# Kernel tuning notes

Measured on AMD Instinct MI355X. Metric: run time of the kernel, lower is better.

## Reference

```python
import jax, jax.numpy as jnp
from jax import lax
import numpy as np

PRE_NMS_TOPN = 6000
POST_NMS_TOPN = 1000  # used as max_output_size_per_class and max_total_size
IOU_THR = 0.7
BATCH = 16
TOTAL_ANCHORS = 147456  # 128*128*9


def setup_inputs() -> dict:
    key = jax.random.key(0)
    k1, k2, k3, k4 = jax.random.split(key, 4)
    B, A = BATCH, TOTAL_ANCHORS
    rpn_bbox_deltas = jax.random.normal(k1, (B, A, 4), jnp.float32) * 0.1
    rpn_labels = jax.random.normal(k2, (B, A), jnp.float32)
    # well-formed anchors in [y1,x1,y2,x2] normalized coords
    tl = jax.random.uniform(k3, (A, 2), jnp.float32, 0.0, 0.9)
    wh = jax.random.uniform(k4, (A, 2), jnp.float32, 0.02, 0.12)
    anchors = jnp.concatenate([tl, tl + wh], axis=-1)
    variances = jnp.array([0.1, 0.1, 0.2, 0.2], jnp.float32)
    return {"rpn_bbox_deltas": rpn_bbox_deltas, "rpn_labels": rpn_labels,
            "anchors": anchors, "variances": variances}


def _decode(anchors, deltas):
    # anchors: (..., A, 4) [y1,x1,y2,x2]; deltas: (..., A, 4) [dy,dx,dh,dw]
    aw = anchors[..., 3] - anchors[..., 1]
    ah = anchors[..., 2] - anchors[..., 0]
    acx = anchors[..., 1] + 0.5 * aw
    acy = anchors[..., 0] + 0.5 * ah
    bw = jnp.exp(deltas[..., 3]) * aw
    bh = jnp.exp(deltas[..., 2]) * ah
    bcx = deltas[..., 1] * aw + acx
    bcy = deltas[..., 0] * ah + acy
    y1 = bcy - 0.5 * bh
    x1 = bcx - 0.5 * bw
    y2 = bh + y1
    x2 = bw + x1
    return jnp.stack([y1, x1, y2, x2], axis=-1)


def _pairwise_iou(b):
    # b: (N, 4) [y1,x1,y2,x2] -> (N, N)
    y1, x1, y2, x2 = b[:, 0], b[:, 1], b[:, 2], b[:, 3]
    area = (y2 - y1) * (x2 - x1)
    iy1 = jnp.maximum(y1[:, None], y1[None, :])
    ix1 = jnp.maximum(x1[:, None], x1[None, :])
    iy2 = jnp.minimum(y2[:, None], y2[None, :])
    ix2 = jnp.minimum(x2[:, None], x2[None, :])
    inter = jnp.maximum(iy2 - iy1, 0.0) * jnp.maximum(ix2 - ix1, 0.0)
    union = area[:, None] + area[None, :] - inter
    return inter / jnp.maximum(union, 1e-9)


def _nms_keep(boxes_sorted):
    # greedy NMS on score-descending boxes; returns bool keep mask (N,)
    n = boxes_sorted.shape[0]
    iou = _pairwise_iou(boxes_sorted)  # (N, N)
    idx = jnp.arange(n)

    def step(suppressed, i):
        kept = jnp.logical_not(suppressed[i])
        suppressed = suppressed | (kept & (iou[i] > IOU_THR) & (idx > i))
        return suppressed, kept

    _, keep = lax.scan(step, jnp.zeros((n,), bool), idx)
    return keep


def _single_image_nms(boxes_sorted, scores_sorted):
    # compact kept entries to the front (score-descending), zero-pad the rest
    keep = _nms_keep(boxes_sorted)
    order = jnp.argsort(jnp.where(keep, 0, 1))  # stable: kept first, in order
    keep_s = keep[order]
    out_boxes = jnp.where(keep_s[:, None], boxes_sorted[order], 0.0)
    out_scores = jnp.where(keep_s, scores_sorted[order], 0.0)
    return out_boxes, out_scores


def _forward(rpn_bbox_deltas, rpn_labels, anchors, variances):
    B = rpn_bbox_deltas.shape[0]
    A = anchors.shape[0]
    deltas = rpn_bbox_deltas.reshape(B, A, 4) * variances  # broadcast (4,)
    scores = jax.nn.softmax(rpn_labels, axis=-1).reshape(B, A)
    boxes = _decode(anchors[None, :, :], deltas)  # (B, A, 4)
    # top-k pre-NMS (topk returns sorted descending -> matches torch sort path)
    top_scores, top_idx = lax.top_k(scores, PRE_NMS_TOPN)
    top_boxes = jnp.take_along_axis(boxes, top_idx[..., None], axis=1)
    # truncate to max_output_size_per_class before NMS (as in the source)
    sb = top_boxes[:, :POST_NMS_TOPN]   # (B, P, 4)
    ss = top_scores[:, :POST_NMS_TOPN]  # (B, P)
    roi_bboxes, roi_scores = jax.vmap(_single_image_nms)(sb, ss)
    return roi_bboxes, roi_scores


def reference(rpn_bbox_deltas, rpn_labels, anchors, variances):
    return _forward(rpn_bbox_deltas, rpn_labels, anchors, variances)
```

## Files before the change

kernel.cpp:

```cpp
#include <hip/hip_runtime.h>

typedef unsigned long long ull;

#define NA 147456
#define NB 16
#define NBINS 16384
#define CAND_CAP 2048
#define SEG 128
#define NPOST 1000

#define OFF_CAND    0
#define OFF_MASK    262144
#define OFF_PART    2310144
#define OFF_SBOX    2312192
#define OFF_SSCORE  2568192

__device__ __forceinline__ unsigned mkey(float f) {
  unsigned u = __float_as_uint(f);
  return u ^ ((unsigned)((int)u >> 31) | 0x80000000u);
}

__global__ __launch_bounds__(1024) void k_select(const float* __restrict__ labels,
                                                 ull* __restrict__ cand,
                                                 float2* __restrict__ partial) {
  int b = blockIdx.x >> 4, blk = blockIdx.x & 15;
  __shared__ unsigned lh[NBINS];
  __shared__ ull sb[256];
  __shared__ float2 wlds[16];
  __shared__ unsigned wsums[16];
  __shared__ unsigned cntT;
  __shared__ int Tlds;
  int tid = threadIdx.x;
  int lane = tid & 63, wid = tid >> 6;
  for (int i = tid; i < NBINS; i += 1024) lh[i] = 0;
  if (tid < 256) sb[tid] = 0ULL;
  if (tid == 0) cntT = 0;
  __syncthreads();

  const int chunk = NA / 16;
  const float4* row4 = (const float4*)(labels + (size_t)b * NA + blk * chunk);

  float4 v0 = row4[tid];
  float4 v1 = row4[tid + 1024];
  bool extra = tid < 256;
  float4 v2 = extra ? row4[tid + 2048] : make_float4(0.f, 0.f, 0.f, 0.f);

  atomicAdd(&lh[mkey(v0.x) >> 18], 1u);
  atomicAdd(&lh[mkey(v0.y) >> 18], 1u);
  atomicAdd(&lh[mkey(v0.z) >> 18], 1u);
  atomicAdd(&lh[mkey(v0.w) >> 18], 1u);
  atomicAdd(&lh[mkey(v1.x) >> 18], 1u);
  atomicAdd(&lh[mkey(v1.y) >> 18], 1u);
  atomicAdd(&lh[mkey(v1.z) >> 18], 1u);
  atomicAdd(&lh[mkey(v1.w) >> 18], 1u);
  if (extra) {
    atomicAdd(&lh[mkey(v2.x) >> 18], 1u);
    atomicAdd(&lh[mkey(v2.y) >> 18], 1u);
    atomicAdd(&lh[mkey(v2.z) >> 18], 1u);
    atomicAdd(&lh[mkey(v2.w) >> 18], 1u);
  }

  float m = fmaxf(fmaxf(fmaxf(v0.x, v0.y), fmaxf(v0.z, v0.w)),
                  fmaxf(fmaxf(v1.x, v1.y), fmaxf(v1.z, v1.w)));
  if (extra) m = fmaxf(m, fmaxf(fmaxf(v2.x, v2.y), fmaxf(v2.z, v2.w)));
  float s = expf(v0.x - m) + expf(v0.y - m) + expf(v0.z - m) + expf(v0.w - m)
          + expf(v1.x - m) + expf(v1.y - m) + expf(v1.z - m) + expf(v1.w - m);
  if (extra)
    s += expf(v2.x - m) + expf(v2.y - m) + expf(v2.z - m) + expf(v2.w - m);
  for (int off = 32; off > 0; off >>= 1) {
    float m2 = __shfl_down(m, off);
    float s2 = __shfl_down(s, off);
    float M = fmaxf(m, m2);
    s = s * expf(m - M) + s2 * expf(m2 - M);
    m = M;
  }
  if (lane == 0) wlds[wid] = make_float2(m, s);
  __syncthreads();
  if (tid == 0) {
    float mm = -INFINITY, ss = 0.f;
    for (int i = 0; i < 16; ++i) {
      float2 p = wlds[i];
      float M = fmaxf(mm, p.x);
      ss = ss * expf(mm - M) + p.y * expf(p.x - M);
      mm = M;
    }
    partial[blockIdx.x] = make_float2(mm, ss);
  }

  unsigned lsum = 0;
  unsigned lbin[16];
#pragma unroll
  for (int q = 0; q < 16; ++q) {
    lbin[q] = lh[NBINS - 1 - (tid * 16 + q)];
    lsum += lbin[q];
  }
  unsigned p = lsum;
  for (int d = 1; d < 64; d <<= 1) {
    unsigned t = __shfl_up(p, d);
    if (lane >= d) p += t;
  }
  if (lane == 63) wsums[wid] = p;
  __syncthreads();
  unsigned wexcl = 0;
#pragma unroll
  for (int w = 0; w < 16; ++w) wexcl += (w < wid) ? wsums[w] : 0u;
  unsigned excl = wexcl + p - lsum;
  unsigned incl = excl + lsum;
  if (excl < SEG && incl >= SEG) {
    unsigned running = excl;
#pragma unroll
    for (int q = 0; q < 16; ++q) {
      unsigned c = lbin[q];
      if (running < SEG && running + c >= SEG) Tlds = NBINS - 1 - (tid * 16 + q);
      running += c;
    }
  }
  __syncthreads();
  unsigned T = (unsigned)Tlds;

  {
    float vals[12] = {v0.x, v0.y, v0.z, v0.w, v1.x, v1.y, v1.z, v1.w,
                      v2.x, v2.y, v2.z, v2.w};
    int nv = extra ? 12 : 8;
    for (int c = 0; c < nv; ++c) {
      unsigned kk = mkey(vals[c]);
      if ((kk >> 18) >= T) {
        unsigned pos = atomicAdd(&cntT, 1u);
        int f4i = (c < 4) ? tid : (c < 8) ? (tid + 1024) : (tid + 2048);
        unsigned idx = (unsigned)(blk * chunk + f4i * 4 + (c & 3));
        if (pos < 256) sb[pos] = ((ull)kk << 32) | (unsigned)~idx;
      }
    }
  }
  __syncthreads();

  if (tid < 64) {
    ull v[4];
#pragma unroll
    for (int r = 0; r < 4; ++r) v[r] = sb[tid * 4 + r];
#pragma unroll
    for (int k = 2; k <= 256; k <<= 1) {
#pragma unroll
      for (int jl = 256; jl > 0; jl >>= 1) {
        int j = jl >> 1;
        if (j == 0 || j >= k) continue;
        if (j >= 4) {
          int lx = j >> 2;
#pragma unroll
          for (int r = 0; r < 4; ++r) {
            ull other = __shfl_xor(v[r], lx);
            int e = tid * 4 + r;
            bool up = (e & k) == 0;
            bool lower = (e & j) == 0;
            bool keep_max = (lower == up);
            bool gt = v[r] > other;
            v[r] = (keep_max == gt) ? v[r] : other;
          }
        } else {
#pragma unroll
          for (int r = 0; r < 4; ++r) {
            int rp = r ^ j;
            if (rp > r) {
              int e = tid * 4 + r;
              bool up = (e & k) == 0;
              ull a = v[r], c2 = v[rp];
              if (up ? (a < c2) : (a > c2)) { v[r] = c2; v[rp] = a; }
            }
          }
        }
      }
    }
    if (tid < 32) {
      ull* cb = cand + (size_t)b * CAND_CAP + blk * SEG;
#pragma unroll
      for (int r = 0; r < 4; ++r) cb[tid * 4 + r] = v[r];
    }
  }
}

__global__ __launch_bounds__(512) void k_rank_emit(const ull* __restrict__ cand,
                                                   const float2* __restrict__ partial,
                                                   const float* __restrict__ labels,
                                                   const float* __restrict__ deltas,
                                                   const float4* __restrict__ anchors,
                                                   const float* __restrict__ variances,
                                                   float4* __restrict__ sboxes,
                                                   float* __restrict__ sscores) {
  int b = blockIdx.x >> 2, part = blockIdx.x & 3;
  __shared__ ull sd[CAND_CAP];
  __shared__ float2 msld;
  for (int i = threadIdx.x; i < CAND_CAP; i += 512)
    sd[i] = cand[(size_t)b * CAND_CAP + i];
  if (threadIdx.x == 0) {
    float m = -INFINITY, s = 0.f;
    for (int i = 0; i < 16; ++i) {
      float2 pp = partial[b * 16 + i];
      float M = fmaxf(m, pp.x);
      s = s * expf(m - M) + pp.y * expf(pp.x - M);
      m = M;
    }
    msld = make_float2(m, s);
  }
  __syncthreads();

  ull x = sd[part * 512 + threadIdx.x];
  int rank = 0;
#pragma unroll
  for (int t = 0; t < 16; ++t) {
    const ull* run = &sd[t << 7];
    int p = 0;
    if (run[p + 63] > x) p += 64;
    if (run[p + 31] > x) p += 32;
    if (run[p + 15] > x) p += 16;
    if (run[p + 7]  > x) p += 8;
    if (run[p + 3]  > x) p += 4;
    if (run[p + 1]  > x) p += 2;
    if (run[p]      > x) p += 1;
    rank += p;
  }
  if (rank >= NPOST) return;

  unsigned idx = ~(unsigned)(x & 0xFFFFFFFFu);
  float2 mt = msld;
  float lab = labels[(size_t)b * NA + idx];
  float score = expf(lab - mt.x) / mt.y;

  float4 an = anchors[idx];
  float aw = an.w - an.y;
  float ah = an.z - an.x;
  float acx = an.y + 0.5f * aw;
  float acy = an.x + 0.5f * ah;
  float4 dl = *(const float4*)(deltas + ((size_t)b * NA + idx) * 4);
  float4 var = *(const float4*)variances;
  float t0 = dl.x * var.x, t1 = dl.y * var.y, t2 = dl.z * var.z, t3 = dl.w * var.w;
  float bw = expf(t3) * aw;
  float bh = expf(t2) * ah;
  float bcx = t1 * aw + acx;
  float bcy = t0 * ah + acy;
  float y1 = bcy - 0.5f * bh, x1 = bcx - 0.5f * bw;
  float y2 = bh + y1, x2 = bw + x1;
  sboxes[(size_t)b * NPOST + rank] = make_float4(y1, x1, y2, x2);
  sscores[(size_t)b * NPOST + rank] = score;
}

__global__ __launch_bounds__(256) void k_mask(const float4* __restrict__ sboxes,
                                              ull* __restrict__ maskT) {
  int b = blockIdx.x / 63, tile = blockIdx.x % 63;
  __shared__ float4 bx[NPOST];
  for (int j = threadIdx.x; j < NPOST; j += 256) bx[j] = sboxes[(size_t)b * NPOST + j];
  __syncthreads();
  int il = threadIdx.x >> 4, w = threadIdx.x & 15;
  int i = tile * 16 + il;
  if (i < NPOST) {
    ull bits = 0;
    if ((w << 6) < i) {
      float4 bi = bx[i];
      float ay1 = bi.x, ax1 = bi.y, ay2 = bi.z, ax2 = bi.w;
      float areai = (ay2 - ay1) * (ax2 - ax1);
      for (int jj = 0; jj < 64; ++jj) {
        int jb = (jj + w) & 63;
        int j = (w << 6) + jb;
        if (j < i) {
          float4 bj = bx[j];
          float areaj = (bj.z - bj.x) * (bj.w - bj.y);
          float iy1 = fmaxf(ay1, bj.x), ix1 = fmaxf(ax1, bj.y);
          float iy2 = fminf(ay2, bj.z), ix2 = fminf(ax2, bj.w);
          float inter = fmaxf(iy2 - iy1, 0.f) * fmaxf(ix2 - ix1, 0.f);
          float uni = areai + areaj - inter;
          float iou = inter / fmaxf(uni, 1e-9f);
          if (iou > 0.7f) bits |= (1ull << jb);
        }
      }
    }
    maskT[((size_t)b * NPOST + i) * 16 + w] = bits;
  }
}

__global__ __launch_bounds__(1024, 1) void k_nms(const ull* __restrict__ maskT,
                                                 const float4* __restrict__ sboxes,
                                                 const float* __restrict__ sscores,
                                                 float* __restrict__ out) {
  int b = blockIdx.x;
  __shared__ ull kept[16], undec[16];
  __shared__ int pref[17];
  int tid = threadIdx.x;
  int wid = tid >> 6, lane = tid & 63;
  const ull* MT = maskT + (size_t)b * NPOST * 16;
  int c = tid < NPOST ? tid : NPOST - 1;
  const ulonglong2* colp = (const ulonglong2*)(MT + (size_t)c * 16);

  ulonglong2 p0 = colp[0], p1 = colp[1], p2 = colp[2], p3 = colp[3];
  ulonglong2 p4 = colp[4], p5 = colp[5], p6 = colp[6], p7 = colp[7];
  ull c0 = p0.x, c1 = p0.y, c2  = p1.x, c3  = p1.y;
  ull c4 = p2.x, c5 = p2.y, c6  = p3.x, c7  = p3.y;
  ull c8 = p4.x, c9 = p4.y, c10 = p5.x, c11 = p5.y;
  ull c12 = p6.x, c13 = p6.y, c14 = p7.x, c15 = p7.y;

  if (tid < 16) {
    kept[tid] = 0ULL;
    undec[tid] = (tid == 15) ? ((1ull << 40) - 1) : ~0ull;
  }
  __syncthreads();

#pragma unroll 1
  for (int round = 0; round < 1024; ++round) {
    ull a  = (c0 & kept[0])  | (c1 & kept[1])  | (c2 & kept[2])  | (c3 & kept[3])
           | (c4 & kept[4])  | (c5 & kept[5])  | (c6 & kept[6])  | (c7 & kept[7])
           | (c8 & kept[8])  | (c9 & kept[9])  | (c10 & kept[10]) | (c11 & kept[11])
           | (c12 & kept[12]) | (c13 & kept[13]) | (c14 & kept[14]) | (c15 & kept[15]);
    ull bb = (c0 & undec[0]) | (c1 & undec[1]) | (c2 & undec[2]) | (c3 & undec[3])
           | (c4 & undec[4]) | (c5 & undec[5]) | (c6 & undec[6]) | (c7 & undec[7])
           | (c8 & undec[8]) | (c9 & undec[9]) | (c10 & undec[10]) | (c11 & undec[11])
           | (c12 & undec[12]) | (c13 & undec[13]) | (c14 & undec[14]) | (c15 & undec[15]);
    bool isundec = ((undec[wid] >> lane) & 1ull) != 0ull;
    bool nr = isundec && (a != 0ull);
    bool nk = isundec && (a == 0ull) && (bb == 0ull);
    ull bk = __ballot(nk);
    ull bd = __ballot(nk || nr);
    __syncthreads();
    if (lane == 0) {
      kept[wid] |= bk;
      undec[wid] &= ~bd;
    }
    int rem = __syncthreads_count((int)(((undec[wid] >> lane) & 1ull) != 0ull));
    if (rem == 0) break;
  }

  if (tid == 0) {
    int a2 = 0;
    for (int w = 0; w < 16; ++w) { pref[w] = a2; a2 += __popcll(kept[w]); }
    pref[16] = a2;
  }
  __syncthreads();

  int total = pref[16];
  float4* ob = (float4*)out;
  float* os = out + (size_t)NB * NPOST * 4;
  for (int r = tid; r < NPOST; r += 1024) {
    if (r >= total) {
      ob[(size_t)b * NPOST + r] = make_float4(0.f, 0.f, 0.f, 0.f);
      os[(size_t)b * NPOST + r] = 0.f;
    }
  }
  for (int r = tid; r < NPOST; r += 1024) {
    int w = r >> 6, bbit = r & 63;
    ull kw = kept[w];
    if ((kw >> bbit) & 1ull) {
      int pos = pref[w] + __popcll(bbit ? (kw & ((1ull << bbit) - 1)) : 0ull);
      ob[(size_t)b * NPOST + pos] = sboxes[(size_t)b * NPOST + r];
      os[(size_t)b * NPOST + pos] = sscores[(size_t)b * NPOST + r];
    }
  }
}

extern "C" void kernel_launch(void* const* d_in, const int* in_sizes, int n_in,
                              void* d_out, int out_size, void* d_ws, size_t ws_size,
                              hipStream_t stream) {
  const float* deltas    = (const float*)d_in[0];
  const float* labels    = (const float*)d_in[1];
  const float* anchors   = (const float*)d_in[2];
  const float* variances = (const float*)d_in[3];

  char* ws = (char*)d_ws;
  ull*     cand    = (ull*)(ws + OFF_CAND);
  ull*     maskT   = (ull*)(ws + OFF_MASK);
  float2*  partial = (float2*)(ws + OFF_PART);
  float4*  sboxes  = (float4*)(ws + OFF_SBOX);
  float*   sscores = (float*)(ws + OFF_SSCORE);

  k_select<<<NB * 16, 1024, 0, stream>>>(labels, cand, partial);
  k_rank_emit<<<NB * 4, 512, 0, stream>>>(cand, partial, labels, deltas,
                                          (const float4*)anchors, variances,
                                          sboxes, sscores);
  k_mask<<<NB * 63, 256, 0, stream>>>(sboxes, maskT);
  k_nms<<<NB, 1024, 0, stream>>>(maskT, sboxes, sscores, (float*)d_out);
}
```

Baseline: 55.22 us.

## Fuse rank-and-emit into select kernel via last-block atomic ticket

Measured after the change: 87.46 us. +58.4%, slower.

```diff
diff --git a/kernel.cpp b/kernel.cpp
--- a/kernel.cpp
+++ b/kernel.cpp
@@ -14,6 +14,7 @@
 #define OFF_PART    2310144
 #define OFF_SBOX    2312192
 #define OFF_SSCORE  2568192
+#define OFF_TICK    2632192
 
 __device__ __forceinline__ unsigned mkey(float f) {
   unsigned u = __float_as_uint(f);
@@ -22,7 +23,13 @@
 
 __global__ __launch_bounds__(1024) void k_select(const float* __restrict__ labels,
                                                  ull* __restrict__ cand,
-                                                 float2* __restrict__ partial) {
+                                                 float2* __restrict__ partial,
+                                                 unsigned* __restrict__ tick,
+                                                 const float* __restrict__ deltas,
+                                                 const float4* __restrict__ anchors,
+                                                 const float* __restrict__ variances,
+                                                 float4* __restrict__ sboxes,
+                                                 float* __restrict__ sscores) {
   int b = blockIdx.x >> 4, blk = blockIdx.x & 15;
   __shared__ unsigned lh[NBINS];
   __shared__ ull sb[256];
@@ -30,6 +37,7 @@
   __shared__ unsigned wsums[16];
   __shared__ unsigned cntT;
   __shared__ int Tlds;
+  __shared__ int fin;
   int tid = threadIdx.x;
   int lane = tid & 63, wid = tid >> 6;
   for (int i = tid; i < NBINS; i += 1024) lh[i] = 0;
@@ -176,71 +184,75 @@
       for (int r = 0; r < 4; ++r) cb[tid * 4 + r] = v[r];
     }
   }
-}
-
-__global__ __launch_bounds__(512) void k_rank_emit(const ull* __restrict__ cand,
-                                                   const float2* __restrict__ partial,
-                                                   const float* __restrict__ labels,
-                                                   const float* __restrict__ deltas,
-                                                   const float4* __restrict__ anchors,
-                                                   const float* __restrict__ variances,
-                                                   float4* __restrict__ sboxes,
-                                                   float* __restrict__ sscores) {
-  int b = blockIdx.x >> 2, part = blockIdx.x & 3;
+
+  __syncthreads();
+  if (tid == 0) {
+    __threadfence();
+    unsigned r = atomicAdd(&tick[b], 1u);
+    fin = (r == 15u);
+  }
+  __syncthreads();
+  if (!fin) return;
+  __threadfence();
+
   __shared__ ull sd[CAND_CAP];
   __shared__ float2 msld;
-  for (int i = threadIdx.x; i < CAND_CAP; i += 512)
+  for (int i = tid; i < CAND_CAP; i += 1024)
     sd[i] = cand[(size_t)b * CAND_CAP + i];
-  if (threadIdx.x == 0) {
-    float m = -INFINITY, s = 0.f;
+  if (tid == 0) {
+    float mm = -INFINITY, ss = 0.f;
     for (int i = 0; i < 16; ++i) {
       float2 pp = partial[b * 16 + i];
-      float M = fmaxf(m, pp.x);
-      s = s * expf(m - M) + pp.y * expf(pp.x - M);
-      m = M;
-    }
-    msld = make_float2(m, s);
-  }
-  __syncthreads();
-
-  ull x = sd[part * 512 + threadIdx.x];
-  int rank = 0;
-#pragma unroll
-  for (int t = 0; t < 16; ++t) {
-    const ull* run = &sd[t << 7];
-    int p = 0;
-    if (run[p + 63] > x) p += 64;
-    if (run[p + 31] > x) p += 32;
-    if (run[p + 15] > x) p += 16;
-    if (run[p + 7]  > x) p += 8;
-    if (run[p + 3]  > x) p += 4;
-    if (run[p + 1]  > x) p += 2;
-    if (run[p]      > x) p += 1;
-    rank += p;
-  }
-  if (rank >= NPOST) return;
-
-  unsigned idx = ~(unsigned)(x & 0xFFFFFFFFu);
-  float2 mt = msld;
-  float lab = labels[(size_t)b * NA + idx];
-  float score = expf(lab - mt.x) / mt.y;
-
-  float4 an = anchors[idx];
-  float aw = an.w - an.y;
-  float ah = an.z - an.x;
-  float acx = an.y + 0.5f * aw;
-  float acy = an.x + 0.5f * ah;
-  float4 dl = *(const float4*)(deltas + ((size_t)b * NA + idx) * 4);
+      float M = fmaxf(mm, pp.x);
+      ss = ss * expf(mm - M) + pp.y * expf(pp.x - M);
+      mm = M;
+    }
+    msld = make_float2(mm, ss);
+  }
+  __syncthreads();
+
   float4 var = *(const float4*)variances;
-  float t0 = dl.x * var.x, t1 = dl.y * var.y, t2 = dl.z * var.z, t3 = dl.w * var.w;
-  float bw = expf(t3) * aw;
-  float bh = expf(t2) * ah;
-  float bcx = t1 * aw + acx;
-  float bcy = t0 * ah + acy;
-  float y1 = bcy - 0.5f * bh, x1 = bcx - 0.5f * bw;
-  float y2 = bh + y1, x2 = bw + x1;
-  sboxes[(size_t)b * NPOST + rank] = make_float4(y1, x1, y2, x2);
-  sscores[(size_t)b * NPOST + rank] = score;
+#pragma unroll
+  for (int half = 0; half < 2; ++half) {
+    ull x = sd[half * 1024 + tid];
+    int rank = 0;
+#pragma unroll
+    for (int t = 0; t < 16; ++t) {
+      const ull* run = &sd[t << 7];
+      int pp = 0;
+      if (run[pp + 63] > x) pp += 64;
+      if (run[pp + 31] > x) pp += 32;
+      if (run[pp + 15] > x) pp += 16;
+      if (run[pp + 7]  > x) pp += 8;
+      if (run[pp + 3]  > x) pp += 4;
+      if (run[pp + 1]  > x) pp += 2;
+      if (run[pp]      > x) pp += 1;
+      rank += pp;
+    }
+    if (rank < NPOST) {
+      unsigned idx = ~(unsigned)(x & 0xFFFFFFFFu);
+      float2 mt = msld;
+      float lab = labels[(size_t)b * NA + idx];
+      float score = expf(lab - mt.x) / mt.y;
+
+      float4 an = anchors[idx];
+      float aw = an.w - an.y;
+      float ah = an.z - an.x;
+      float acx = an.y + 0.5f * aw;
+      float acy = an.x + 0.5f * ah;
+      float4 dl = *(const float4*)(deltas + ((size_t)b * NA + idx) * 4);
+      float t0 = dl.x * var.x, t1 = dl.y * var.y;
+      float t2 = dl.z * var.z, t3 = dl.w * var.w;
+      float bw = expf(t3) * aw;
+      float bh = expf(t2) * ah;
+      float bcx = t1 * aw + acx;
+      float bcy = t0 * ah + acy;
+      float y1 = bcy - 0.5f * bh, x1 = bcx - 0.5f * bw;
+      float y2 = bh + y1, x2 = bw + x1;
+      sboxes[(size_t)b * NPOST + rank] = make_float4(y1, x1, y2, x2);
+      sscores[(size_t)b * NPOST + rank] = score;
+    }
+  }
 }
 
 __global__ __launch_bounds__(256) void k_mask(const float4* __restrict__ sboxes,
@@ -362,16 +374,17 @@
   const float* variances = (const float*)d_in[3];
 
   char* ws = (char*)d_ws;
-  ull*     cand    = (ull*)(ws + OFF_CAND);
-  ull*     maskT   = (ull*)(ws + OFF_MASK);
-  float2*  partial = (float2*)(ws + OFF_PART);
-  float4*  sboxes  = (float4*)(ws + OFF_SBOX);
-  float*   sscores = (float*)(ws + OFF_SSCORE);
-
-  k_select<<<NB * 16, 1024, 0, stream>>>(labels, cand, partial);
-  k_rank_emit<<<NB * 4, 512, 0, stream>>>(cand, partial, labels, deltas,
-                                          (const float4*)anchors, variances,
-                                          sboxes, sscores);
+  ull*      cand    = (ull*)(ws + OFF_CAND);
+  ull*      maskT   = (ull*)(ws + OFF_MASK);
+  float2*   partial = (float2*)(ws + OFF_PART);
+  float4*   sboxes  = (float4*)(ws + OFF_SBOX);
+  float*    sscores = (float*)(ws + OFF_SSCORE);
+  unsigned* tick    = (unsigned*)(ws + OFF_TICK);
+
+  hipMemsetAsync(ws + OFF_TICK, 0, 64, stream);
+  k_select<<<NB * 16, 1024, 0, stream>>>(labels, cand, partial, tick,
+                                         deltas, (const float4*)anchors,
+                                         variances, sboxes, sscores);
   k_mask<<<NB * 63, 256, 0, stream>>>(sboxes, maskT);
   k_nms<<<NB, 1024, 0, stream>>>(maskT, sboxes, sscores, (float*)d_out);
 }
```
